# Kernel tuning notes

Hardware: AMD Instinct MI355X
Metric: run time of the kernel (lower is better)

The kernel has to match this reference:

```python
import jax, jax.numpy as jnp
import numpy as np

B, L, H, NH = 8, 384, 512, 8
DH = H // NH
MAX_SEQ_LEN = 384


def setup_inputs() -> dict:
    key = jax.random.key(0)
    ks = jax.random.split(key, 16)
    s = 0.02
    seq_len = jnp.concatenate([
        jnp.array([L], dtype=jnp.int32),
        jax.random.randint(ks[3], (B - 1,), L // 2, L + 1, dtype=jnp.int32),
    ])
    return {
        "key": jax.random.normal(ks[0], (B, L, H), jnp.float32),
        "query": jax.random.normal(ks[1], (B, L, H), jnp.float32),
        "value": jax.random.normal(ks[2], (B, L, H), jnp.float32),
        "seq_len": seq_len,
        "pe": jax.random.normal(ks[4], (2 * MAX_SEQ_LEN + 1, H), jnp.float32) * s,
        "Wk": jax.random.normal(ks[5], (H, H), jnp.float32) * s,
        "bk": jnp.zeros((H,), jnp.float32),
        "Wq": jax.random.normal(ks[6], (H, H), jnp.float32) * s,
        "bq": jnp.zeros((H,), jnp.float32),
        "Wv": jax.random.normal(ks[7], (H, H), jnp.float32) * s,
        "bv": jnp.zeros((H,), jnp.float32),
        "Wr": jax.random.normal(ks[8], (H, H), jnp.float32) * s,
        "br": jnp.zeros((H,), jnp.float32),
        "u_bias": jax.random.normal(ks[9], (NH, DH), jnp.float32) * s,
        "v_bias": jax.random.normal(ks[10], (NH, DH), jnp.float32) * s,
        "Wff": jax.random.normal(ks[11], (H, H), jnp.float32) * s,
        "bff": jnp.zeros((H,), jnp.float32),
    }


def reference(key, query, value, seq_len, pe, Wk, bk, Wq, bq, Wv, bv, Wr, br, u_bias, v_bias, Wff, bff):
    # relative distances: rel[i, j] = j - i, in [-(L-1), L-1]
    rel = jnp.arange(L)[None, :] - jnp.arange(L)[:, None]          # [L, L]
    rpe = pe[rel + MAX_SEQ_LEN]                                    # [L, L, H]

    k = (key @ Wk.T + bk).reshape(B, L, NH, DH)
    q = (query @ Wq.T + bq).reshape(B, L, NH, DH)
    v = (value @ Wv.T + bv).reshape(B, L, NH, DH)
    rpe = (rpe @ Wr.T + br).reshape(L, L, NH, DH)

    # Transformer-XL score terms
    A = jnp.einsum('bihd,bjhd->bhij', q, k)                        # content-content
    Bt = jnp.einsum('bihd,ijhd->bhij', q, rpe)                     # content-position
    C = jnp.einsum('hd,bjhd->bhj', u_bias, k)[:, :, None, :]       # global content bias
    Dt = jnp.einsum('hd,ijhd->hij', v_bias, rpe)[None]             # global position bias

    scores = (A + Bt + C + Dt) / jnp.sqrt(jnp.float32(DH))
    key_mask = jnp.arange(L)[None, :] < seq_len[:, None]           # [B, L]
    scores = jnp.where(key_mask[:, None, None, :], scores, -1e15)
    attn = jax.nn.softmax(scores, axis=-1)                         # [B, NH, L, L]

    out = jnp.einsum('bhij,bjhd->bihd', attn, v).reshape(B, L, H)
    return out @ Wff.T + bff
```

## Files before the change

### kernel.cpp

```cpp
#include <hip/hip_runtime.h>
#include <hip/hip_bf16.h>

#define B_  8
#define L_  384
#define H_  512
#define NH_ 8
#define DH_ 64
#define RRM 768

typedef short bf16x8 __attribute__((ext_vector_type(8)));
typedef float f32x4  __attribute__((ext_vector_type(4)));
#define MFMA_BF16 __builtin_amdgcn_mfma_f32_16x16x32_bf16

static __device__ __forceinline__ unsigned short f2bf(float f) {
    unsigned u = __builtin_bit_cast(unsigned, f);
    u += 0x7fffu + ((u >> 16) & 1u);
    return (unsigned short)(u >> 16);
}
static __device__ __forceinline__ float bf2f(unsigned short s) {
    unsigned u = ((unsigned)s) << 16;
    return __builtin_bit_cast(float, u);
}

typedef unsigned int u32;
static __device__ __forceinline__ void glds16(const void* g, void* l) {
    __builtin_amdgcn_global_load_lds(
        (const __attribute__((address_space(1))) u32*)g,
        (__attribute__((address_space(3))) u32*)l, 16, 0, 0);
}

struct CvtArgs {
    const float* src[9];
    unsigned short* dst[9];
    int nchunks[9];
};
__global__ __launch_bounds__(256) void cvt_kernel(CvtArgs a) {
    int chunk = blockIdx.x;
    int r = 0;
    while (r < 8 && chunk >= a.nchunks[r]) { chunk -= a.nchunks[r]; r++; }
    const float4 v = ((const float4*)a.src[r])[chunk * 256 + threadIdx.x];
    ushort4 o;
    o.x = f2bf(v.x); o.y = f2bf(v.y); o.z = f2bf(v.z); o.w = f2bf(v.w);
    ((ushort4*)a.dst[r])[chunk * 256 + threadIdx.x] = o;
}

template <bool IS_FF>
__global__ __launch_bounds__(256) void gemm_nt(
    const unsigned short* __restrict__ A0, const unsigned short* __restrict__ A1,
    const unsigned short* __restrict__ A2, const unsigned short* __restrict__ A3,
    const unsigned short* __restrict__ A4,
    const unsigned short* __restrict__ W0, const unsigned short* __restrict__ W1,
    const unsigned short* __restrict__ W2, const unsigned short* __restrict__ W3,
    const unsigned short* __restrict__ W4,
    const float* __restrict__ b0, const float* __restrict__ b1,
    const float* __restrict__ b2, const float* __restrict__ b3,
    const float* __restrict__ b4,
    const float* __restrict__ ub, const float* __restrict__ vbias,
    unsigned short* __restrict__ qu, unsigned short* __restrict__ qv,
    unsigned short* __restrict__ kb, unsigned short* __restrict__ vT,
    unsigned short* __restrict__ rp, float* __restrict__ ff) {

    const int z = IS_FF ? 4 : blockIdx.z;
    if (!IS_FF && z == 3 && blockIdx.y >= 12) return;
    const unsigned short* A = z == 0 ? A0 : z == 1 ? A1 : z == 2 ? A2 : z == 3 ? A3 : A4;
    const unsigned short* W = z == 0 ? W0 : z == 1 ? W1 : z == 2 ? W2 : z == 3 ? W3 : W4;
    const float* bias       = z == 0 ? b0 : z == 1 ? b1 : z == 2 ? b2 : z == 3 ? b3 : b4;

    __shared__ unsigned short AsF[2 * 64 * 64];
    __shared__ unsigned short BsF[2 * 64 * 64];

    const int tid = threadIdx.x;
    const int w = tid >> 6, lane = tid & 63;
    const int quad = lane >> 4, lm = lane & 15;
    const int wr = (w & 1) * 32, wc = (w >> 1) * 32;

    const int sr = lane >> 3, sj = lane & 7;
    const unsigned short* ga = A + (size_t)(blockIdx.y * 64 + w * 16 + sr) * 512 + (sj ^ sr) * 8;
    const unsigned short* gb = W + (size_t)(blockIdx.x * 64 + w * 16 + sr) * 512 + (sj ^ sr) * 8;

    auto stage = [&](int kc, int buf) {
        #pragma unroll
        for (int t = 0; t < 2; ++t) {
            int off = buf * 4096 + (w * 16 + t * 8) * 64;
            off = __builtin_amdgcn_readfirstlane(off);
            glds16(ga + kc * 64 + t * 8 * 512, &AsF[off]);
            glds16(gb + kc * 64 + t * 8 * 512, &BsF[off]);
        }
    };

    f32x4 acc[2][2] = {};
    stage(0, 0);
    for (int kc = 0; kc < 8; ++kc) {
        __syncthreads();
        const int buf = kc & 1;
        if (kc < 7) stage(kc + 1, buf ^ 1);
        const int base = buf * 4096;
        #pragma unroll
        for (int ks = 0; ks < 2; ++ks) {
            const int s = (((ks * 4 + quad) ^ (lm & 7))) * 8;
            bf16x8 a0 = *(const bf16x8*)&AsF[base + (wr + lm) * 64 + s];
            bf16x8 a1 = *(const bf16x8*)&AsF[base + (wr + 16 + lm) * 64 + s];
            bf16x8 w0 = *(const bf16x8*)&BsF[base + (wc + lm) * 64 + s];
            bf16x8 w1 = *(const bf16x8*)&BsF[base + (wc + 16 + lm) * 64 + s];
            acc[0][0] = MFMA_BF16(a0, w0, acc[0][0], 0, 0, 0);
            acc[0][1] = MFMA_BF16(a0, w1, acc[0][1], 0, 0, 0);
            acc[1][0] = MFMA_BF16(a1, w0, acc[1][0], 0, 0, 0);
            acc[1][1] = MFMA_BF16(a1, w1, acc[1][1], 0, 0, 0);
        }
    }

    #pragma unroll
    for (int si = 0; si < 2; ++si) {
        #pragma unroll
        for (int sj2 = 0; sj2 < 2; ++sj2) {
            #pragma unroll
            for (int reg = 0; reg < 4; ++reg) {
                const int r = blockIdx.y * 64 + wr + si * 16 + quad * 4 + reg;
                const int c = blockIdx.x * 64 + wc + sj2 * 16 + lm;
                const float val = acc[si][sj2][reg] + bias[c];
                if (IS_FF) {
                    ff[r * 512 + c] = val;
                } else if (z == 0) {
                    const int bb = r / L_, ii = r - bb * L_;
                    const int h = c >> 6, d = c & 63;
                    const int idx = ((bb * NH_ + h) * L_ + ii) * DH_ + d;
                    qu[idx] = f2bf((val + ub[c]) * 0.125f);
                    qv[idx] = f2bf((val + vbias[c]) * 0.125f);
                } else if (z == 1) {
                    const int bb = r / L_, ii = r - bb * L_;
                    const int h = c >> 6, d = c & 63;
                    kb[((bb * NH_ + h) * L_ + ii) * DH_ + d] = f2bf(val);
                } else if (z == 2) {
                    const int bb = r / L_, ii = r - bb * L_;
                    const int h = c >> 6, d = c & 63;
                    vT[((bb * NH_ + h) * DH_ + d) * L_ + ii] = f2bf(val);
                } else {
                    rp[r * 512 + c] = f2bf(val);
                }
            }
        }
    }
}

#define BTSTR 424
__global__ __launch_bounds__(256) void attn_fused(
    const unsigned short* __restrict__ qu, const unsigned short* __restrict__ qv,
    const unsigned short* __restrict__ kbf, const unsigned short* __restrict__ vT,
    const unsigned short* __restrict__ rp, const int* __restrict__ seq_len,
    unsigned short* __restrict__ Obf) {
    __shared__ __align__(16) unsigned short BtP[32 * BTSTR];
    __shared__ float mx_red[32][2];
    __shared__ float sm_red[32][2];
    const int lane = threadIdx.x & 63, wv = threadIdx.x >> 6;
    const int quad = lane >> 4, lm = lane & 15;
    const int bh = blockIdx.y, b = bh >> 3, h = bh & 7;
    const int i0 = blockIdx.x * 32;
    const int sl = seq_len[b];
    const int msub = wv & 1, nh = wv >> 1;
    const int m_lo = 353 - i0;
    const int i_fr = i0 + msub * 16 + lm;

    {
        const unsigned short* qvr = qv + (size_t)(bh * L_ + i_fr) * DH_;
        const bf16x8 av0 = *(const bf16x8*)(qvr + quad * 8);
        const bf16x8 av1 = *(const bf16x8*)(qvr + 32 + quad * 8);
        #pragma unroll
        for (int ns = 0; ns < 13; ++ns) {
            const int ntl = nh * 208 + ns * 16;
            if (ntl <= sl + 30) {
                const int n = ntl + lm;
                const unsigned short* rrow = rp + (size_t)(m_lo + n) * 512 + h * 64;
                f32x4 bacc = {};
                bacc = MFMA_BF16(av0, *(const bf16x8*)(rrow + quad * 8), bacc, 0, 0, 0);
                bacc = MFMA_BF16(av1, *(const bf16x8*)(rrow + 32 + quad * 8), bacc, 0, 0, 0);
                #pragma unroll
                for (int reg = 0; reg < 4; ++reg) {
                    const int il = msub * 16 + quad * 4 + reg;
                    BtP[il * BTSTR + n] = f2bf(bacc[reg]);
                }
            }
        }
    }
    const unsigned short* qur = qu + (size_t)(bh * L_ + i_fr) * DH_;
    const bf16x8 au0 = *(const bf16x8*)(qur + quad * 8);
    const bf16x8 au1 = *(const bf16x8*)(qur + 32 + quad * 8);
    __syncthreads();

    f32x4 sc[12];
    #pragma unroll
    for (int ns = 0; ns < 12; ++ns) {
        const int jt = nh * 192 + ns * 16;
        if (jt < sl) {
            const unsigned short* krow = kbf + (size_t)(bh * L_ + jt + lm) * DH_;
            f32x4 a = {};
            a = MFMA_BF16(au0, *(const bf16x8*)(krow + quad * 8), a, 0, 0, 0);
            a = MFMA_BF16(au1, *(const bf16x8*)(krow + 32 + quad * 8), a, 0, 0, 0);
            sc[ns] = a;
        } else {
            sc[ns] = f32x4{-1e30f, -1e30f, -1e30f, -1e30f};
        }
    }
    const int jbase = nh * 192 + lm;
    #pragma unroll
    for (int ns = 0; ns < 12; ++ns) {
        const int j = jbase + ns * 16;
        #pragma unroll
        for (int reg = 0; reg < 4; ++reg) {
            const int il = msub * 16 + quad * 4 + reg;
            float val = -1e30f;
            if (j < sl) val = sc[ns][reg] + bf2f(BtP[il * BTSTR + (j - il + 31)]);
            sc[ns][reg] = val;
        }
    }

    const int il0 = msub * 16 + quad * 4;
    float mx4[4], sm4[4], inv4[4];
    #pragma unroll
    for (int reg = 0; reg < 4; ++reg) {
        float m = sc[0][reg];
        #pragma unroll
        for (int ns = 1; ns < 12; ++ns) m = fmaxf(m, sc[ns][reg]);
        #pragma unroll
        for (int o = 1; o < 16; o <<= 1) m = fmaxf(m, __shfl_xor(m, o));
        mx4[reg] = m;
    }
    if (lm == 0) {
        #pragma unroll
        for (int reg = 0; reg < 4; ++reg) mx_red[il0 + reg][nh] = mx4[reg];
    }
    __syncthreads();
    #pragma unroll
    for (int reg = 0; reg < 4; ++reg)
        mx4[reg] = fmaxf(mx_red[il0 + reg][0], mx_red[il0 + reg][1]);
    #pragma unroll
    for (int reg = 0; reg < 4; ++reg) sm4[reg] = 0.f;
    #pragma unroll
    for (int ns = 0; ns < 12; ++ns) {
        #pragma unroll
        for (int reg = 0; reg < 4; ++reg) {
            const float e = __expf(sc[ns][reg] - mx4[reg]);
            sc[ns][reg] = e;
            sm4[reg] += e;
        }
    }
    #pragma unroll
    for (int reg = 0; reg < 4; ++reg) {
        float s = sm4[reg];
        #pragma unroll
        for (int o = 1; o < 16; o <<= 1) s += __shfl_xor(s, o);
        sm4[reg] = s;
    }
    if (lm == 0) {
        #pragma unroll
        for (int reg = 0; reg < 4; ++reg) sm_red[il0 + reg][nh] = sm4[reg];
    }
    __syncthreads();
    #pragma unroll
    for (int reg = 0; reg < 4; ++reg)
        inv4[reg] = 1.f / (sm_red[il0 + reg][0] + sm_red[il0 + reg][1]);

    #pragma unroll
    for (int ns = 0; ns < 12; ++ns) {
        const int j = jbase + ns * 16;
        #pragma unroll
        for (int reg = 0; reg < 4; ++reg)
            BtP[(il0 + reg) * BTSTR + j] = f2bf(sc[ns][reg] * inv4[reg]);
    }
    __syncthreads();

    {
        const int pr = msub * 16 + lm;
        const int nkc = (sl + 31) >> 5;
        f32x4 oacc[2] = {};
        for (int kc = 0; kc < nkc; ++kc) {
            const bf16x8 af = *(const bf16x8*)&BtP[pr * BTSTR + kc * 32 + quad * 8];
            #pragma unroll
            for (int t = 0; t < 2; ++t) {
                const int n = nh * 32 + t * 16 + lm;
                const unsigned short* vrow = vT + (size_t)(bh * DH_ + n) * L_ + kc * 32 + quad * 8;
                oacc[t] = MFMA_BF16(af, *(const bf16x8*)(vrow), oacc[t], 0, 0, 0);
            }
        }
        #pragma unroll
        for (int t = 0; t < 2; ++t) {
            #pragma unroll
            for (int reg = 0; reg < 4; ++reg) {
                const int i = i0 + msub * 16 + quad * 4 + reg;
                const int d = nh * 32 + t * 16 + lm;
                Obf[(size_t)(b * L_ + i) * H_ + h * DH_ + d] = f2bf(oacc[t][reg]);
            }
        }
    }
}

extern "C" void kernel_launch(void* const* d_in, const int* in_sizes, int n_in,
                              void* d_out, int out_size, void* d_ws, size_t ws_size,
                              hipStream_t stream) {
    const float* key    = (const float*)d_in[0];
    const float* query  = (const float*)d_in[1];
    const float* value  = (const float*)d_in[2];
    const int*   seqlen = (const int*)d_in[3];
    const float* pe     = (const float*)d_in[4];
    const float* Wk     = (const float*)d_in[5];
    const float* bk     = (const float*)d_in[6];
    const float* Wq     = (const float*)d_in[7];
    const float* bq     = (const float*)d_in[8];
    const float* Wv     = (const float*)d_in[9];
    const float* bv     = (const float*)d_in[10];
    const float* Wr     = (const float*)d_in[11];
    const float* br     = (const float*)d_in[12];
    const float* u_bias = (const float*)d_in[13];
    const float* v_bias = (const float*)d_in[14];
    const float* Wff    = (const float*)d_in[15];
    const float* bff    = (const float*)d_in[16];

    const size_t nTok = (size_t)B_ * L_ * H_;
    const size_t nPe  = (size_t)RRM * H_;
    const size_t nW   = (size_t)H_ * H_;
    unsigned short* p  = (unsigned short*)d_ws;
    unsigned short* qbf  = p; p += nTok;
    unsigned short* kin  = p; p += nTok;
    unsigned short* vin  = p; p += nTok;
    unsigned short* pebf = p; p += nPe;
    unsigned short* Wqb  = p; p += nW;
    unsigned short* Wkb  = p; p += nW;
    unsigned short* Wvb  = p; p += nW;
    unsigned short* Wrb  = p; p += nW;
    unsigned short* Wffb = p; p += nW;
    unsigned short* qu   = p; p += nTok;
    unsigned short* qv   = p; p += nTok;
    unsigned short* kb   = p; p += nTok;
    unsigned short* vT   = p; p += nTok;
    unsigned short* rp   = p; p += nPe + 512;
    unsigned short* Obf  = qbf;

    CvtArgs ca;
    ca.src[0] = query;  ca.dst[0] = qbf;  ca.nchunks[0] = 1536;
    ca.src[1] = key;    ca.dst[1] = kin;  ca.nchunks[1] = 1536;
    ca.src[2] = value;  ca.dst[2] = vin;  ca.nchunks[2] = 1536;
    ca.src[3] = pe;     ca.dst[3] = pebf; ca.nchunks[3] = 384;
    ca.src[4] = Wq;     ca.dst[4] = Wqb;  ca.nchunks[4] = 256;
    ca.src[5] = Wk;     ca.dst[5] = Wkb;  ca.nchunks[5] = 256;
    ca.src[6] = Wv;     ca.dst[6] = Wvb;  ca.nchunks[6] = 256;
    ca.src[7] = Wr;     ca.dst[7] = Wrb;  ca.nchunks[7] = 256;
    ca.src[8] = Wff;    ca.dst[8] = Wffb; ca.nchunks[8] = 256;
    cvt_kernel<<<6272, 256, 0, stream>>>(ca);

    gemm_nt<false><<<dim3(8, 48, 4), 256, 0, stream>>>(
         qbf, kin, vin, pebf, nullptr,
         Wqb, Wkb, Wvb, Wrb, nullptr,
         bq, bk, bv, br, nullptr,
         u_bias, v_bias,
         qu, qv, kb, vT, rp,
         nullptr);

    attn_fused<<<dim3(L_ / 32, B_ * NH_), 256, 0, stream>>>(
        qu, qv, kb, vT, rp, seqlen, Obf);

    gemm_nt<true><<<dim3(8, 48, 1), 256, 0, stream>>>(
         nullptr, nullptr, nullptr, nullptr, Obf,
         nullptr, nullptr, nullptr, nullptr, Wffb,
         nullptr, nullptr, nullptr, nullptr, bff,
         nullptr, nullptr,
         nullptr, nullptr, nullptr, nullptr, nullptr,
         (float*)d_out);
}
```

Measured before the change: 161.0 us.

## Fuse all stages into one persistent cooperative kernel with grid syncs

Replaces the four separate launches (convert, QKVR projection GEMM, attention, output GEMM) with a single cooperative persistent kernel of 512 blocks. Each phase loops over its work items, and the phases are separated by grid-wide barriers. The aim is to remove launch overhead and inter-kernel gaps, at the cost of grid.sync stalls and tail imbalance inside each phase. If the cooperative launch fails, it falls back to four separate persistent kernels.

```diff
diff --git a/kernel.cpp b/kernel.cpp
--- a/kernel.cpp
+++ b/kernel.cpp
@@ -1,5 +1,7 @@
 #include <hip/hip_runtime.h>
 #include <hip/hip_bf16.h>
+#include <hip/hip_cooperative_groups.h>
+namespace cg = cooperative_groups;
 
 #define B_  8
 #define L_  384
@@ -21,7 +23,6 @@
     unsigned u = ((unsigned)s) << 16;
     return __builtin_bit_cast(float, u);
 }
-
 typedef unsigned int u32;
 static __device__ __forceinline__ void glds16(const void* g, void* l) {
     __builtin_amdgcn_global_load_lds(
@@ -29,62 +30,59 @@
         (__attribute__((address_space(3))) u32*)l, 16, 0, 0);
 }
 
-struct CvtArgs {
-    const float* src[9];
-    unsigned short* dst[9];
-    int nchunks[9];
+struct KArgs {
+    const float *query, *key, *value, *pe;
+    const float *Wq, *Wk, *Wv, *Wr, *Wff;
+    const float *bq, *bk, *bv, *br, *bff, *ub, *vb;
+    const int* seqlen;
+    unsigned short *qbf, *kin, *vin, *pebf;
+    unsigned short *Wqb, *Wkb, *Wvb, *Wrb, *Wffb;
+    unsigned short *qu, *qv, *kb, *vT, *rp, *Obf;
+    float* out;
 };
-__global__ __launch_bounds__(256) void cvt_kernel(CvtArgs a) {
-    int chunk = blockIdx.x;
-    int r = 0;
-    while (r < 8 && chunk >= a.nchunks[r]) { chunk -= a.nchunks[r]; r++; }
-    const float4 v = ((const float4*)a.src[r])[chunk * 256 + threadIdx.x];
-    ushort4 o;
-    o.x = f2bf(v.x); o.y = f2bf(v.y); o.z = f2bf(v.z); o.w = f2bf(v.w);
-    ((ushort4*)a.dst[r])[chunk * 256 + threadIdx.x] = o;
-}
-
-template <bool IS_FF>
-__global__ __launch_bounds__(256) void gemm_nt(
-    const unsigned short* __restrict__ A0, const unsigned short* __restrict__ A1,
-    const unsigned short* __restrict__ A2, const unsigned short* __restrict__ A3,
-    const unsigned short* __restrict__ A4,
-    const unsigned short* __restrict__ W0, const unsigned short* __restrict__ W1,
-    const unsigned short* __restrict__ W2, const unsigned short* __restrict__ W3,
-    const unsigned short* __restrict__ W4,
-    const float* __restrict__ b0, const float* __restrict__ b1,
-    const float* __restrict__ b2, const float* __restrict__ b3,
-    const float* __restrict__ b4,
-    const float* __restrict__ ub, const float* __restrict__ vbias,
-    unsigned short* __restrict__ qu, unsigned short* __restrict__ qv,
-    unsigned short* __restrict__ kb, unsigned short* __restrict__ vT,
-    unsigned short* __restrict__ rp, float* __restrict__ ff) {
-
-    const int z = IS_FF ? 4 : blockIdx.z;
-    if (!IS_FF && z == 3 && blockIdx.y >= 12) return;
-    const unsigned short* A = z == 0 ? A0 : z == 1 ? A1 : z == 2 ? A2 : z == 3 ? A3 : A4;
-    const unsigned short* W = z == 0 ? W0 : z == 1 ? W1 : z == 2 ? W2 : z == 3 ? W3 : W4;
-    const float* bias       = z == 0 ? b0 : z == 1 ? b1 : z == 2 ? b2 : z == 3 ? b3 : b4;
-
-    __shared__ unsigned short AsF[2 * 64 * 64];
-    __shared__ unsigned short BsF[2 * 64 * 64];
+
+static __device__ __forceinline__ void phase1(const KArgs& a) {
+    const float* src[9] = {a.query, a.key, a.value, a.pe, a.Wq, a.Wk, a.Wv, a.Wr, a.Wff};
+    unsigned short* dst[9] = {a.qbf, a.kin, a.vin, a.pebf, a.Wqb, a.Wkb, a.Wvb, a.Wrb, a.Wffb};
+    const int nch[9] = {1536, 1536, 1536, 384, 256, 256, 256, 256, 256};
+    for (int c = blockIdx.x; c < 6272; c += gridDim.x) {
+        int cc = c, r = 0;
+        while (r < 8 && cc >= nch[r]) { cc -= nch[r]; ++r; }
+        const float4 v = ((const float4*)src[r])[cc * 256 + threadIdx.x];
+        ushort4 o;
+        o.x = f2bf(v.x); o.y = f2bf(v.y); o.z = f2bf(v.z); o.w = f2bf(v.w);
+        ((ushort4*)dst[r])[cc * 256 + threadIdx.x] = o;
+    }
+}
+
+static __device__ void gemm_tile(const KArgs& a, int z, int bx, int by,
+                                 unsigned short* sm) {
+    const unsigned short *A, *W; const float* bias;
+    switch (z) {
+        case 0: A = a.qbf;  W = a.Wqb;  bias = a.bq;  break;
+        case 1: A = a.kin;  W = a.Wkb;  bias = a.bk;  break;
+        case 2: A = a.vin;  W = a.Wvb;  bias = a.bv;  break;
+        case 3: A = a.pebf; W = a.Wrb;  bias = a.br;  break;
+        default: A = a.Obf; W = a.Wffb; bias = a.bff; break;
+    }
+    unsigned short* AsF = sm;
+    unsigned short* BsF = sm + 8192;
 
     const int tid = threadIdx.x;
     const int w = tid >> 6, lane = tid & 63;
     const int quad = lane >> 4, lm = lane & 15;
     const int wr = (w & 1) * 32, wc = (w >> 1) * 32;
-
     const int sr = lane >> 3, sj = lane & 7;
-    const unsigned short* ga = A + (size_t)(blockIdx.y * 64 + w * 16 + sr) * 512 + (sj ^ sr) * 8;
-    const unsigned short* gb = W + (size_t)(blockIdx.x * 64 + w * 16 + sr) * 512 + (sj ^ sr) * 8;
+    const unsigned short* ga = A + (size_t)(by * 64 + w * 16 + sr) * 512 + (sj ^ sr) * 8;
+    const unsigned short* gb = W + (size_t)(bx * 64 + w * 16 + sr) * 512 + (sj ^ sr) * 8;
 
     auto stage = [&](int kc, int buf) {
         #pragma unroll
-        for (int t = 0; t < 2; ++t) {
-            int off = buf * 4096 + (w * 16 + t * 8) * 64;
+        for (int t2 = 0; t2 < 2; ++t2) {
+            int off = buf * 4096 + (w * 16 + t2 * 8) * 64;
             off = __builtin_amdgcn_readfirstlane(off);
-            glds16(ga + kc * 64 + t * 8 * 512, &AsF[off]);
-            glds16(gb + kc * 64 + t * 8 * 512, &BsF[off]);
+            glds16(ga + kc * 64 + t2 * 8 * 512, &AsF[off]);
+            glds16(gb + kc * 64 + t2 * 8 * 512, &BsF[off]);
         }
     };
 
@@ -115,53 +113,62 @@
         for (int sj2 = 0; sj2 < 2; ++sj2) {
             #pragma unroll
             for (int reg = 0; reg < 4; ++reg) {
-                const int r = blockIdx.y * 64 + wr + si * 16 + quad * 4 + reg;
-                const int c = blockIdx.x * 64 + wc + sj2 * 16 + lm;
+                const int r = by * 64 + wr + si * 16 + quad * 4 + reg;
+                const int c = bx * 64 + wc + sj2 * 16 + lm;
                 const float val = acc[si][sj2][reg] + bias[c];
-                if (IS_FF) {
-                    ff[r * 512 + c] = val;
+                if (z == 4) {
+                    a.out[r * 512 + c] = val;
                 } else if (z == 0) {
                     const int bb = r / L_, ii = r - bb * L_;
                     const int h = c >> 6, d = c & 63;
                     const int idx = ((bb * NH_ + h) * L_ + ii) * DH_ + d;
-                    qu[idx] = f2bf((val + ub[c]) * 0.125f);
-                    qv[idx] = f2bf((val + vbias[c]) * 0.125f);
+                    a.qu[idx] = f2bf((val + a.ub[c]) * 0.125f);
+                    a.qv[idx] = f2bf((val + a.vb[c]) * 0.125f);
                 } else if (z == 1) {
                     const int bb = r / L_, ii = r - bb * L_;
                     const int h = c >> 6, d = c & 63;
-                    kb[((bb * NH_ + h) * L_ + ii) * DH_ + d] = f2bf(val);
+                    a.kb[((bb * NH_ + h) * L_ + ii) * DH_ + d] = f2bf(val);
                 } else if (z == 2) {
                     const int bb = r / L_, ii = r - bb * L_;
                     const int h = c >> 6, d = c & 63;
-                    vT[((bb * NH_ + h) * DH_ + d) * L_ + ii] = f2bf(val);
+                    a.vT[((bb * NH_ + h) * DH_ + d) * L_ + ii] = f2bf(val);
                 } else {
-                    rp[r * 512 + c] = f2bf(val);
+                    a.rp[r * 512 + c] = f2bf(val);
                 }
             }
         }
     }
 }
 
+static __device__ __forceinline__ void phase2(const KArgs& a, unsigned short* sm) {
+    for (int t = blockIdx.x; t < 1248; t += gridDim.x) {
+        int z, bx, by;
+        if (t < 1152) { z = t / 384; const int rem = t % 384; by = rem >> 3; bx = rem & 7; }
+        else          { z = 3;       const int rem = t - 1152; by = rem >> 3; bx = rem & 7; }
+        gemm_tile(a, z, bx, by, sm);
+    }
+}
+static __device__ __forceinline__ void phase4(const KArgs& a, unsigned short* sm) {
+    for (int t = blockIdx.x; t < 384; t += gridDim.x)
+        gemm_tile(a, 4, t & 7, t >> 3, sm);
+}
+
 #define BTSTR 424
-__global__ __launch_bounds__(256) void attn_fused(
-    const unsigned short* __restrict__ qu, const unsigned short* __restrict__ qv,
-    const unsigned short* __restrict__ kbf, const unsigned short* __restrict__ vT,
-    const unsigned short* __restrict__ rp, const int* __restrict__ seq_len,
-    unsigned short* __restrict__ Obf) {
-    __shared__ __align__(16) unsigned short BtP[32 * BTSTR];
-    __shared__ float mx_red[32][2];
-    __shared__ float sm_red[32][2];
+static __device__ void attn_unit(const KArgs& a, int i_t, int bh,
+                                 unsigned short* BtP,
+                                 float (*mx_red)[2], float (*sm_red)[2]) {
+    __syncthreads();
     const int lane = threadIdx.x & 63, wv = threadIdx.x >> 6;
     const int quad = lane >> 4, lm = lane & 15;
-    const int bh = blockIdx.y, b = bh >> 3, h = bh & 7;
-    const int i0 = blockIdx.x * 32;
-    const int sl = seq_len[b];
+    const int b = bh >> 3, h = bh & 7;
+    const int i0 = i_t * 32;
+    const int sl = a.seqlen[b];
     const int msub = wv & 1, nh = wv >> 1;
     const int m_lo = 353 - i0;
     const int i_fr = i0 + msub * 16 + lm;
 
     {
-        const unsigned short* qvr = qv + (size_t)(bh * L_ + i_fr) * DH_;
+        const unsigned short* qvr = a.qv + (size_t)(bh * L_ + i_fr) * DH_;
         const bf16x8 av0 = *(const bf16x8*)(qvr + quad * 8);
         const bf16x8 av1 = *(const bf16x8*)(qvr + 32 + quad * 8);
         #pragma unroll
@@ -169,7 +176,7 @@
             const int ntl = nh * 208 + ns * 16;
             if (ntl <= sl + 30) {
                 const int n = ntl + lm;
-                const unsigned short* rrow = rp + (size_t)(m_lo + n) * 512 + h * 64;
+                const unsigned short* rrow = a.rp + (size_t)(m_lo + n) * 512 + h * 64;
                 f32x4 bacc = {};
                 bacc = MFMA_BF16(av0, *(const bf16x8*)(rrow + quad * 8), bacc, 0, 0, 0);
                 bacc = MFMA_BF16(av1, *(const bf16x8*)(rrow + 32 + quad * 8), bacc, 0, 0, 0);
@@ -181,7 +188,7 @@
             }
         }
     }
-    const unsigned short* qur = qu + (size_t)(bh * L_ + i_fr) * DH_;
+    const unsigned short* qur = a.qu + (size_t)(bh * L_ + i_fr) * DH_;
     const bf16x8 au0 = *(const bf16x8*)(qur + quad * 8);
     const bf16x8 au1 = *(const bf16x8*)(qur + 32 + quad * 8);
     __syncthreads();
@@ -191,11 +198,11 @@
     for (int ns = 0; ns < 12; ++ns) {
         const int jt = nh * 192 + ns * 16;
         if (jt < sl) {
-            const unsigned short* krow = kbf + (size_t)(bh * L_ + jt + lm) * DH_;
-            f32x4 a = {};
-            a = MFMA_BF16(au0, *(const bf16x8*)(krow + quad * 8), a, 0, 0, 0);
-            a = MFMA_BF16(au1, *(const bf16x8*)(krow + 32 + quad * 8), a, 0, 0, 0);
-            sc[ns] = a;
+            const unsigned short* krow = a.kb + (size_t)(bh * L_ + jt + lm) * DH_;
+            f32x4 acc = {};
+            acc = MFMA_BF16(au0, *(const bf16x8*)(krow + quad * 8), acc, 0, 0, 0);
+            acc = MFMA_BF16(au1, *(const bf16x8*)(krow + 32 + quad * 8), acc, 0, 0, 0);
+            sc[ns] = acc;
         } else {
             sc[ns] = f32x4{-1e30f, -1e30f, -1e30f, -1e30f};
         }
@@ -277,7 +284,7 @@
             #pragma unroll
             for (int t = 0; t < 2; ++t) {
                 const int n = nh * 32 + t * 16 + lm;
-                const unsigned short* vrow = vT + (size_t)(bh * DH_ + n) * L_ + kc * 32 + quad * 8;
+                const unsigned short* vrow = a.vT + (size_t)(bh * DH_ + n) * L_ + kc * 32 + quad * 8;
                 oacc[t] = MFMA_BF16(af, *(const bf16x8*)(vrow), oacc[t], 0, 0, 0);
             }
         }
@@ -287,81 +294,98 @@
             for (int reg = 0; reg < 4; ++reg) {
                 const int i = i0 + msub * 16 + quad * 4 + reg;
                 const int d = nh * 32 + t * 16 + lm;
-                Obf[(size_t)(b * L_ + i) * H_ + h * DH_ + d] = f2bf(oacc[t][reg]);
+                a.Obf[(size_t)(b * L_ + i) * H_ + h * DH_ + d] = f2bf(oacc[t][reg]);
             }
         }
     }
+}
+
+static __device__ __forceinline__ void phase3(const KArgs& a, unsigned short* sm,
+                                              float (*mx_red)[2], float (*sm_red)[2]) {
+    for (int u = blockIdx.x; u < 768; u += gridDim.x)
+        attn_unit(a, u % 12, u / 12, sm, mx_red, sm_red);
+}
+
+__global__ __launch_bounds__(256, 2) void fused_all(KArgs a) {
+    __shared__ __align__(16) unsigned short smem[16384];
+    __shared__ float mx_red[32][2], sm_red[32][2];
+    cg::grid_group grid = cg::this_grid();
+
+    phase1(a);
+    __threadfence(); grid.sync();
+    phase2(a, smem);
+    __threadfence(); grid.sync();
+    phase3(a, smem, mx_red, sm_red);
+    __threadfence(); grid.sync();
+    phase4(a, smem);
+}
+
+__global__ __launch_bounds__(256, 2) void ph1_k(KArgs a) { phase1(a); }
+__global__ __launch_bounds__(256, 2) void ph2_k(KArgs a) {
+    __shared__ __align__(16) unsigned short smem[16384];
+    phase2(a, smem);
+}
+__global__ __launch_bounds__(256, 2) void ph3_k(KArgs a) {
+    __shared__ __align__(16) unsigned short smem[16384];
+    __shared__ float mx_red[32][2], sm_red[32][2];
+    phase3(a, smem, mx_red, sm_red);
+}
+__global__ __launch_bounds__(256, 2) void ph4_k(KArgs a) {
+    __shared__ __align__(16) unsigned short smem[16384];
+    phase4(a, smem);
 }
 
 extern "C" void kernel_launch(void* const* d_in, const int* in_sizes, int n_in,
                               void* d_out, int out_size, void* d_ws, size_t ws_size,
                               hipStream_t stream) {
-    const float* key    = (const float*)d_in[0];
-    const float* query  = (const float*)d_in[1];
-    const float* value  = (const float*)d_in[2];
-    const int*   seqlen = (const int*)d_in[3];
-    const float* pe     = (const float*)d_in[4];
-    const float* Wk     = (const float*)d_in[5];
-    const float* bk     = (const float*)d_in[6];
-    const float* Wq     = (const float*)d_in[7];
-    const float* bq     = (const float*)d_in[8];
-    const float* Wv     = (const float*)d_in[9];
-    const float* bv     = (const float*)d_in[10];
-    const float* Wr     = (const float*)d_in[11];
-    const float* br     = (const float*)d_in[12];
-    const float* u_bias = (const float*)d_in[13];
-    const float* v_bias = (const float*)d_in[14];
-    const float* Wff    = (const float*)d_in[15];
-    const float* bff    = (const float*)d_in[16];
+    KArgs ka;
+    ka.key    = (const float*)d_in[0];
+    ka.query  = (const float*)d_in[1];
+    ka.value  = (const float*)d_in[2];
+    ka.seqlen = (const int*)d_in[3];
+    ka.pe     = (const float*)d_in[4];
+    ka.Wk     = (const float*)d_in[5];
+    ka.bk     = (const float*)d_in[6];
+    ka.Wq     = (const float*)d_in[7];
+    ka.bq     = (const float*)d_in[8];
+    ka.Wv     = (const float*)d_in[9];
+    ka.bv     = (const float*)d_in[10];
+    ka.Wr     = (const float*)d_in[11];
+    ka.br     = (const float*)d_in[12];
+    ka.ub     = (const float*)d_in[13];
+    ka.vb     = (const float*)d_in[14];
+    ka.Wff    = (const float*)d_in[15];
+    ka.bff    = (const float*)d_in[16];
+    ka.out    = (float*)d_out;
 
     const size_t nTok = (size_t)B_ * L_ * H_;
     const size_t nPe  = (size_t)RRM * H_;
     const size_t nW   = (size_t)H_ * H_;
-    unsigned short* p  = (unsigned short*)d_ws;
-    unsigned short* qbf  = p; p += nTok;
-    unsigned short* kin  = p; p += nTok;
-    unsigned short* vin  = p; p += nTok;
-    unsigned short* pebf = p; p += nPe;
-    unsigned short* Wqb  = p; p += nW;
-    unsigned short* Wkb  = p; p += nW;
-    unsigned short* Wvb  = p; p += nW;
-    unsigned short* Wrb  = p; p += nW;
-    unsigned short* Wffb = p; p += nW;
-    unsigned short* qu   = p; p += nTok;
-    unsigned short* qv   = p; p += nTok;
-    unsigned short* kb   = p; p += nTok;
-    unsigned short* vT   = p; p += nTok;
-    unsigned short* rp   = p; p += nPe + 512;
-    unsigned short* Obf  = qbf;
-
-    CvtArgs ca;
-    ca.src[0] = query;  ca.dst[0] = qbf;  ca.nchunks[0] = 1536;
-    ca.src[1] = key;    ca.dst[1] = kin;  ca.nchunks[1] = 1536;
-    ca.src[2] = value;  ca.dst[2] = vin;  ca.nchunks[2] = 1536;
-    ca.src[3] = pe;     ca.dst[3] = pebf; ca.nchunks[3] = 384;
-    ca.src[4] = Wq;     ca.dst[4] = Wqb;  ca.nchunks[4] = 256;
-    ca.src[5] = Wk;     ca.dst[5] = Wkb;  ca.nchunks[5] = 256;
-    ca.src[6] = Wv;     ca.dst[6] = Wvb;  ca.nchunks[6] = 256;
-    ca.src[7] = Wr;     ca.dst[7] = Wrb;  ca.nchunks[7] = 256;
-    ca.src[8] = Wff;    ca.dst[8] = Wffb; ca.nchunks[8] = 256;
-    cvt_kernel<<<6272, 256, 0, stream>>>(ca);
-
-    gemm_nt<false><<<dim3(8, 48, 4), 256, 0, stream>>>(
-         qbf, kin, vin, pebf, nullptr,
-         Wqb, Wkb, Wvb, Wrb, nullptr,
-         bq, bk, bv, br, nullptr,
-         u_bias, v_bias,
-         qu, qv, kb, vT, rp,
-         nullptr);
-
-    attn_fused<<<dim3(L_ / 32, B_ * NH_), 256, 0, stream>>>(
-        qu, qv, kb, vT, rp, seqlen, Obf);
-
-    gemm_nt<true><<<dim3(8, 48, 1), 256, 0, stream>>>(
-         nullptr, nullptr, nullptr, nullptr, Obf,
-         nullptr, nullptr, nullptr, nullptr, Wffb,
-         nullptr, nullptr, nullptr, nullptr, bff,
-         nullptr, nullptr,
-         nullptr, nullptr, nullptr, nullptr, nullptr,
-         (float*)d_out);
-}
+    unsigned short* p = (unsigned short*)d_ws;
+    ka.qbf  = p; p += nTok;
+    ka.kin  = p; p += nTok;
+    ka.vin  = p; p += nTok;
+    ka.pebf = p; p += nPe;
+    ka.Wqb  = p; p += nW;
+    ka.Wkb  = p; p += nW;
+    ka.Wvb  = p; p += nW;
+    ka.Wrb  = p; p += nW;
+    ka.Wffb = p; p += nW;
+    ka.qu   = p; p += nTok;
+    ka.qv   = p; p += nTok;
+    ka.kb   = p; p += nTok;
+    ka.vT   = p; p += nTok;
+    ka.rp   = p; p += nPe + 512;
+    ka.Obf  = ka.qbf;
+
+    void* params[] = { &ka };
+    hipError_t e = hipLaunchCooperativeKernel((const void*)fused_all, dim3(512),
+                                              dim3(256), params, 0, stream);
+    if (e != hipSuccess) {
+        (void)hipGetLastError();
+        ph1_k<<<512, 256, 0, stream>>>(ka);
+        ph2_k<<<512, 256, 0, stream>>>(ka);
+        ph3_k<<<768, 256, 0, stream>>>(ka);
+        ph4_k<<<384, 256, 0, stream>>>(ka);
+    }
+}
```

Result: slower. 543.6 us (+237.7%).
